# Kernel tuning notes

Measured on AMD Instinct MI355X. Metric: run time of the kernel, lower is better.

Reference implementation:

```python
import jax, jax.numpy as jnp
import numpy as np

FG_THRESH = 0.5
BG_HI = 0.5
BG_LO = 0.0
CLS_LAMBDA = 1.0
BBOX2D_LAMBDA = 1.0
BBOX3D_LAMBDA = 1.0

A, FH, FW, STRIDE = 36, 32, 106, 16  # 36*32*106 = 122112 anchors
B, G, NC = 4, 64, 4


def _smooth_l1(x):
    ax = jnp.abs(x)
    return jnp.where(ax < 1.0, 0.5 * ax * ax, ax - 0.5)


def setup_inputs() -> dict:
    rng = np.random.RandomState(0)
    # anchors: [x1,y1,x2,y2, z, w3d, h3d, l3d, ry], centered at origin
    ws = rng.uniform(16, 256, A).astype(np.float32)
    hs = rng.uniform(16, 256, A).astype(np.float32)
    anchors = np.zeros((A, 9), np.float32)
    anchors[:, 0] = -ws / 2; anchors[:, 1] = -hs / 2
    anchors[:, 2] = ws / 2;  anchors[:, 3] = hs / 2
    anchors[:, 4] = rng.uniform(5, 50, A)
    anchors[:, 5:8] = rng.uniform(1, 5, (A, 3))
    anchors[:, 8] = rng.uniform(-np.pi, np.pi, A)
    # rois = anchors tiled over the feature grid (locate_anchors), col 4 = anchor idx
    sx, sy = np.meshgrid(np.arange(FW) * STRIDE, np.arange(FH) * STRIDE)
    shifts = np.stack([sx.ravel(), sy.ravel(), sx.ravel(), sy.ravel()], 1).astype(np.float32)
    N = FH * FW * A
    rois = np.zeros((N, 5), np.float32)
    rois[:, :4] = (shifts[:, None, :] + anchors[None, :, :4]).reshape(-1, 4)
    rois[:, 4] = np.tile(np.arange(A), FH * FW)
    # GT 2D boxes (x1,y1,x2,y2) inside the 1696x512 image
    gcx = rng.uniform(0, FW * STRIDE, (B, G)); gcy = rng.uniform(0, FH * STRIDE, (B, G))
    gw = rng.uniform(30, 200, (B, G)); gh = rng.uniform(30, 200, (B, G))
    gt_boxes = np.stack([gcx - gw / 2, gcy - gh / 2, gcx + gw / 2, gcy + gh / 2], -1).astype(np.float32)
    # GT 3D: projected 3D center (u,v), z, w3d, h3d, l3d, ry
    gt_boxes_3d = np.stack([
        gcx, gcy,
        rng.uniform(5, 50, (B, G)),
        rng.uniform(1, 5, (B, G)), rng.uniform(1, 5, (B, G)), rng.uniform(1, 5, (B, G)),
        rng.uniform(-np.pi, np.pi, (B, G)),
    ], -1).astype(np.float32)
    gt_labels = rng.randint(1, NC, (B, G)).astype(np.int32)
    bbox_means = (rng.randn(1, 11) * 0.01).astype(np.float32)
    bbox_stds = (0.1 + rng.rand(1, 11) * 0.2).astype(np.float32)
    key = jax.random.key(0)
    k1, k2, k3, k4 = jax.random.split(key, 4)
    return {
        "cls": jax.random.normal(k1, (B, N, NC), jnp.float32),
        "prob": jax.random.uniform(k2, (B, N, NC), jnp.float32),
        "bbox_2d": 0.1 * jax.random.normal(k3, (B, N, 4), jnp.float32),
        "bbox_3d": 0.1 * jax.random.normal(k4, (B, N, 7), jnp.float32),
        "rois": jnp.asarray(rois),
        "anchors": jnp.asarray(anchors),
        "bbox_means": jnp.asarray(bbox_means),
        "bbox_stds": jnp.asarray(bbox_stds),
        "gt_boxes": jnp.asarray(gt_boxes),
        "gt_boxes_3d": jnp.asarray(gt_boxes_3d),
        "gt_labels": jnp.asarray(gt_labels),
    }


def _loss(cls, prob, bbox_2d, bbox_3d, rois, anchors, bbox_means, bbox_stds,
          gt_boxes, gt_boxes_3d, gt_labels):
    # anchor geometry (the +1.0 convention matches the torch code)
    widths = rois[:, 2] - rois[:, 0] + 1.0          # [N]
    heights = rois[:, 3] - rois[:, 1] + 1.0
    ctr_x = rois[:, 0] + 0.5 * widths
    ctr_y = rois[:, 1] + 0.5 * heights
    aidx = rois[:, 4].astype(jnp.int32)
    src = anchors[aidx]                             # [N,9] gathered anchors

    # IoU between every roi and every GT: [B,N,G]
    rx1 = rois[None, :, None, 0]; ry1 = rois[None, :, None, 1]
    rx2 = rois[None, :, None, 2]; ry2 = rois[None, :, None, 3]
    gx1 = gt_boxes[:, None, :, 0]; gy1 = gt_boxes[:, None, :, 1]
    gx2 = gt_boxes[:, None, :, 2]; gy2 = gt_boxes[:, None, :, 3]
    iw = jnp.clip(jnp.minimum(rx2, gx2) - jnp.maximum(rx1, gx1) + 1.0, 0.0)
    ih = jnp.clip(jnp.minimum(ry2, gy2) - jnp.maximum(ry1, gy1) + 1.0, 0.0)
    inter = iw * ih
    area_r = (rx2 - rx1 + 1.0) * (ry2 - ry1 + 1.0)
    area_g = (gx2 - gx1 + 1.0) * (gy2 - gy1 + 1.0)
    ols = inter / (area_r + area_g - inter)         # [B,N,G]

    best_iou = jnp.max(ols, axis=-1)                # [B,N]
    best_gt = jnp.argmax(ols, axis=-1)              # [B,N]

    fg = best_iou >= FG_THRESH
    bg = (best_iou < BG_HI) & (best_iou >= BG_LO) & (~fg)

    matched_lbl = jnp.take_along_axis(gt_labels, best_gt, axis=1)   # [B,N]
    labels = jnp.where(fg, matched_lbl, 0)

    gb = jnp.take_along_axis(gt_boxes, best_gt[..., None], axis=1)  # [B,N,4]
    gw = gb[..., 2] - gb[..., 0] + 1.0
    gh = gb[..., 3] - gb[..., 1] + 1.0
    gcx = gb[..., 0] + 0.5 * gw
    gcy = gb[..., 1] + 0.5 * gh
    t2d = jnp.stack([
        (gcx - ctr_x) / widths,
        (gcy - ctr_y) / heights,
        jnp.log(gw / widths),
        jnp.log(gh / heights),
    ], -1)
    t2d = (t2d - bbox_means[0, 0:4]) / bbox_stds[0, 0:4]

    g3 = jnp.take_along_axis(gt_boxes_3d, best_gt[..., None], axis=1)  # [B,N,7]
    t3d = jnp.stack([
        (g3[..., 0] - ctr_x) / widths,
        (g3[..., 1] - ctr_y) / heights,
        g3[..., 2] - src[:, 4],
        jnp.log(g3[..., 3] / src[:, 5]),
        jnp.log(g3[..., 4] / src[:, 6]),
        jnp.log(g3[..., 5] / src[:, 7]),
        g3[..., 6] - src[:, 8],
    ], -1)
    t3d = (t3d - bbox_means[0, 4:11]) / bbox_stds[0, 4:11]

    # ---- losses
    w_fg = fg.astype(cls.dtype)
    n_fg = jnp.maximum(jnp.sum(w_fg), 1.0)
    loss_b2d = jnp.sum(jnp.sum(_smooth_l1(bbox_2d - t2d), -1) * w_fg) / n_fg
    loss_b3d = jnp.sum(jnp.sum(_smooth_l1(bbox_3d - t3d), -1) * w_fg) / n_fg

    w_cls = (fg | bg).astype(cls.dtype)
    logp = jax.nn.log_softmax(cls, axis=-1)
    ce = -jnp.take_along_axis(logp, labels[..., None], axis=-1)[..., 0]
    loss_cls = jnp.sum(ce * w_cls) / jnp.maximum(jnp.sum(w_cls), 1.0)

    return CLS_LAMBDA * loss_cls + BBOX2D_LAMBDA * loss_b2d + BBOX3D_LAMBDA * loss_b3d


def reference(cls, prob, bbox_2d, bbox_3d, rois, anchors, bbox_means, bbox_stds,
              gt_boxes, gt_boxes_3d, gt_labels):
    return _loss(cls, prob, bbox_2d, bbox_3d, rois, anchors, bbox_means, bbox_stds,
                 gt_boxes, gt_boxes_3d, gt_labels)
```

## Files before the change

### kernel.cpp

```cpp
#include <hip/hip_runtime.h>
#include <math.h>

#define AA 36
#define FWW 106
#define NTOT 122112
#define BB 4
#define GG 64
#define STRIDE_PX 16
#define FBIG 3.402823466e+38f

constexpr int BLOCK = 512;
constexpr int NW    = BLOCK / 64;
constexpr int BLOCKS_PER_B = (NTOT + BLOCK - 1) / BLOCK;
constexpr int NBLK = BB * BLOCKS_PER_B;

__device__ __forceinline__ float smooth_l1(float x) {
    float ax = fabsf(x);
    return (ax < 1.0f) ? 0.5f * ax * ax : ax - 0.5f;
}
__device__ __forceinline__ float frcp(float x) { return __builtin_amdgcn_rcpf(x); }

#define DPP_SELF(x, ctrl, rm)                                                 \
    __int_as_float(__builtin_amdgcn_update_dpp(__float_as_int(x),             \
                   __float_as_int(x), ctrl, rm, 0xf, false))
#define DPP_ZERO(x, ctrl, rm)                                                 \
    __int_as_float(__builtin_amdgcn_update_dpp(0, __float_as_int(x),          \
                   ctrl, rm, 0xf, true))
#define RLANE_F(v, l) __int_as_float(__builtin_amdgcn_readlane(__float_as_int(v), (l)))

__device__ __forceinline__ float wave_sum64(float x) {
    x += DPP_ZERO(x, 0x111, 0xf);
    x += DPP_ZERO(x, 0x112, 0xf);
    x += DPP_ZERO(x, 0x114, 0xf);
    x += DPP_ZERO(x, 0x118, 0xf);
    x += DPP_ZERO(x, 0x142, 0xa);
    x += DPP_ZERO(x, 0x143, 0xc);
    return x;
}
__device__ __forceinline__ float wave_min64_bcast(float x) {
    x = fminf(x, DPP_SELF(x, 0x111, 0xf));
    x = fminf(x, DPP_SELF(x, 0x112, 0xf));
    x = fminf(x, DPP_SELF(x, 0x114, 0xf));
    x = fminf(x, DPP_SELF(x, 0x118, 0xf));
    x = fminf(x, DPP_SELF(x, 0x142, 0xa));
    x = fminf(x, DPP_SELF(x, 0x143, 0xc));
    return RLANE_F(x, 63);
}
__device__ __forceinline__ float wave_max64_bcast(float x) {
    x = fmaxf(x, DPP_SELF(x, 0x111, 0xf));
    x = fmaxf(x, DPP_SELF(x, 0x112, 0xf));
    x = fmaxf(x, DPP_SELF(x, 0x114, 0xf));
    x = fmaxf(x, DPP_SELF(x, 0x118, 0xf));
    x = fmaxf(x, DPP_SELF(x, 0x142, 0xa));
    x = fmaxf(x, DPP_SELF(x, 0x143, 0xc));
    return RLANE_F(x, 63);
}

__global__ __launch_bounds__(BLOCK) void rpn_loss_main(
    const float* __restrict__ cls,
    const float* __restrict__ bbox2d,
    const float* __restrict__ bbox3d,
    const float* __restrict__ anchors,
    const float* __restrict__ means,
    const float* __restrict__ stds,
    const float* __restrict__ gt_boxes,
    const float* __restrict__ gt3d,
    const int*   __restrict__ gt_labels,
    float4* __restrict__ part)
{
    __shared__ float4 s_red[NW];

    const int tid  = threadIdx.x;
    const int lane = tid & 63;
    const int wv   = tid >> 6;
    const int b    = blockIdx.x / BLOCKS_PER_B;
    const int bpos = blockIdx.x % BLOCKS_PER_B;
    const int n0   = bpos * BLOCK;
    const int n    = n0 + tid;
    const bool valid = (n < NTOT);

    const float4* __restrict__ gtb = reinterpret_cast<const float4*>(gt_boxes) + b * GG;

    const size_t row = (size_t)b * NTOT + n;
    float4 c = make_float4(0.f, 0.f, 0.f, 0.f);
    if (valid) c = reinterpret_cast<const float4*>(cls)[row];

    const int aidx  = n % AA;
    const int shift = n / AA;
    const float sx  = (float)((shift % FWW) * STRIDE_PX);
    const float sy  = (float)((shift / FWW) * STRIDE_PX);
    const float a0 = anchors[aidx * 9 + 0];
    const float a1 = anchors[aidx * 9 + 1];
    const float a2 = anchors[aidx * 9 + 2];
    const float a3 = anchors[aidx * 9 + 3];
    const float aw  = a2 - a0 + 1.0f;
    const float ah  = a3 - a1 + 1.0f;
    const float x1  = sx + a0;
    const float y1  = sy + a1;
    const float x2p = x1 + aw;
    const float y2p = y1 + ah;
    const float ar  = aw * ah;

    const float4 gt   = gtb[lane];
    const float  gz1p = gt.z + 1.0f;
    const float  gw1p = gt.w + 1.0f;
    const float  ag   = (gz1p - gt.x) * (gw1p - gt.y);

    float e0 = FBIG, e1 = FBIG, e2 = -FBIG, e3 = -FBIG, ew = 0.f, eh = 0.f, eS = FBIG;
    if (lane < AA) {
        const float b0 = anchors[lane * 9 + 0];
        const float b1 = anchors[lane * 9 + 1];
        const float b2 = anchors[lane * 9 + 2];
        const float b3 = anchors[lane * 9 + 3];
        e0 = b0; e1 = b1; e2 = b2; e3 = b3;
        ew = b2 - b0 + 1.0f;
        eh = b3 - b1 + 1.0f;
        eS = ew * eh;
    }
    const float mnx = wave_min64_bcast(e0);
    const float mny = wave_min64_bcast(e1);
    const float mxx = wave_max64_bcast(e2);
    const float mxy = wave_max64_bcast(e3);
    const float mxw = wave_max64_bcast(ew) + 1.0f;
    const float mxh = wave_max64_bcast(eh) + 1.0f;
    const float mnS = wave_min64_bcast(eS);

    const int nlast = (n0 + BLOCK - 1 < NTOT) ? (n0 + BLOCK - 1) : (NTOT - 1);
    const int s0  = n0 / AA,  s1  = nlast / AA;
    const int sy0 = s0 / FWW, sy1 = s1 / FWW;
    float fxA0, fxA1, fyA, fxB0, fxB1, fyB;
    if (sy0 == sy1) {
        fxA0 = (float)((s0 % FWW) * STRIDE_PX); fxA1 = (float)((s1 % FWW) * STRIDE_PX);
        fyA  = (float)(sy0 * STRIDE_PX);
        fxB0 = fxA0; fxB1 = fxA1; fyB = fyA;
    } else {
        fxA0 = (float)((s0 % FWW) * STRIDE_PX); fxA1 = (float)((FWW - 1) * STRIDE_PX);
        fyA  = (float)(sy0 * STRIDE_PX);
        fxB0 = 0.0f;                            fxB1 = (float)((s1 % FWW) * STRIDE_PX);
        fyB  = (float)(sy1 * STRIDE_PX);
    }

    float iwA = fminf(fxA1 + mxx + 1.0f, gz1p) - fmaxf(fxA0 + mnx, gt.x);
    iwA = fmaxf(fminf(iwA, mxw), 0.0f);
    float ihA = fminf(fyA + mxy + 1.0f, gw1p) - fmaxf(fyA + mny, gt.y);
    ihA = fmaxf(fminf(ihA, mxh), 0.0f);
    bool pass = (3.0f * iwA * ihA >= mnS + ag);
    float iwB = fminf(fxB1 + mxx + 1.0f, gz1p) - fmaxf(fxB0 + mnx, gt.x);
    iwB = fmaxf(fminf(iwB, mxw), 0.0f);
    float ihB = fminf(fyB + mxy + 1.0f, gw1p) - fmaxf(fyB + mny, gt.y);
    ihB = fmaxf(fminf(ihB, mxh), 0.0f);
    pass = pass || (3.0f * iwB * ihB >= mnS + ag);

    unsigned long long m = __ballot(pass);

    const float lse = __logf(__expf(c.x) + __expf(c.y) + __expf(c.z) + __expf(c.w));

    float bi = 0.0f, bS = 1.0f;
    int   bk = 0;
    while (m) {
        const int g = (int)__builtin_ctzll(m);
        m &= (m - 1ull);
        const float gxs = RLANE_F(gt.x,  g);
        const float gys = RLANE_F(gt.y,  g);
        const float gzs = RLANE_F(gz1p,  g);
        const float gws = RLANE_F(gw1p,  g);
        const float ags = RLANE_F(ag,    g);
        const float iw = fminf(x2p, gzs) - fmaxf(x1, gxs);
        const float ih = fmaxf(fminf(y2p, gws) - fmaxf(y1, gys), 0.0f);
        const float inter = iw * ih;
        const float S     = ar + ags;
        const bool upd = inter * bS > bi * S;
        bi = upd ? inter : bi;
        bS = upd ? S     : bS;
        bk = upd ? g     : bk;
    }
    const bool fg = valid && (3.0f * bi >= bS);

    int label = 0;
    if (fg) label = gt_labels[b * GG + bk];
    const float csel = (label == 0) ? c.x : (label == 1) ? c.y :
                       (label == 2) ? c.z : c.w;
    const float ce = valid ? (lse - csel) : 0.0f;

    float l23 = 0.0f;
    if (fg) {
        const float cx  = x1 + 0.5f * aw;
        const float cy  = y1 + 0.5f * ah;
        const float rw  = frcp(aw);
        const float rh  = frcp(ah);
        const float4 gq = gtb[bk];
        const float gw_ = gq.z - gq.x + 1.0f;
        const float gh_ = gq.w - gq.y + 1.0f;
        const float gcx = gq.x + 0.5f * gw_;
        const float gcy = gq.y + 0.5f * gh_;
        float t2[4];
        t2[0] = (gcx - cx) * rw;
        t2[1] = (gcy - cy) * rh;
        t2[2] = __logf(gw_ * rw);
        t2[3] = __logf(gh_ * rh);
        const float4 p2 = reinterpret_cast<const float4*>(bbox2d)[row];
        const float p2a[4] = {p2.x, p2.y, p2.z, p2.w};
        #pragma unroll
        for (int k = 0; k < 4; ++k)
            l23 += smooth_l1(p2a[k] - (t2[k] - means[k]) * frcp(stds[k]));

        const float an4 = anchors[aidx * 9 + 4];
        const float an5 = anchors[aidx * 9 + 5];
        const float an6 = anchors[aidx * 9 + 6];
        const float an7 = anchors[aidx * 9 + 7];
        const float an8 = anchors[aidx * 9 + 8];
        const float* g3 = gt3d + ((size_t)b * GG + bk) * 7;
        float t3[7];
        t3[0] = (g3[0] - cx) * rw;
        t3[1] = (g3[1] - cy) * rh;
        t3[2] = g3[2] - an4;
        t3[3] = __logf(g3[3] * frcp(an5));
        t3[4] = __logf(g3[4] * frcp(an6));
        t3[5] = __logf(g3[5] * frcp(an7));
        t3[6] = g3[6] - an8;
        const float* p3 = bbox3d + row * 7;
        #pragma unroll
        for (int k = 0; k < 7; ++k)
            l23 += smooth_l1(p3[k] - (t3[k] - means[4 + k]) * frcp(stds[4 + k]));
    }

    const float vce = wave_sum64(ce);
    const float vl  = wave_sum64(l23);
    const float nfgw = (float)__popcll(__ballot(fg));
    if (lane == 63) s_red[wv] = make_float4(vce, vl, nfgw, 0.f);
    __syncthreads();
    if (tid < NW) {
        float4 p = s_red[tid];
        #pragma unroll
        for (int mm = 1; mm < NW; mm <<= 1) {
            p.x += __shfl_xor(p.x, mm, 64);
            p.y += __shfl_xor(p.y, mm, 64);
            p.z += __shfl_xor(p.z, mm, 64);
        }
        if (tid == 0) part[blockIdx.x] = p;
    }
}

__global__ __launch_bounds__(256) void rpn_loss_fin(
    const float4* __restrict__ part, float* __restrict__ out)
{
    __shared__ float4 sh[4];
    float ce = 0.f, l23 = 0.f, nfg = 0.f;
    for (int i = threadIdx.x; i < NBLK; i += 256) {
        const float4 p = part[i];
        ce += p.x; l23 += p.y; nfg += p.z;
    }
    ce  = wave_sum64(ce);
    l23 = wave_sum64(l23);
    nfg = wave_sum64(nfg);
    const int lane = threadIdx.x & 63;
    const int wv   = threadIdx.x >> 6;
    if (lane == 63) sh[wv] = make_float4(ce, l23, nfg, 0.f);
    __syncthreads();
    if (threadIdx.x == 0) {
        float a = 0.f, l = 0.f, g = 0.f;
        #pragma unroll
        for (int i = 0; i < 4; ++i) { a += sh[i].x; l += sh[i].y; g += sh[i].z; }
        out[0] = a / (float)((size_t)BB * NTOT) + l / fmaxf(g, 1.0f);
    }
}

extern "C" void kernel_launch(void* const* d_in, const int* in_sizes, int n_in,
                              void* d_out, int out_size, void* d_ws, size_t ws_size,
                              hipStream_t stream) {
    const float* cls     = (const float*)d_in[0];
    const float* bbox2d  = (const float*)d_in[2];
    const float* bbox3d  = (const float*)d_in[3];
    const float* anchors = (const float*)d_in[5];
    const float* means   = (const float*)d_in[6];
    const float* stds    = (const float*)d_in[7];
    const float* gtb     = (const float*)d_in[8];
    const float* gt3     = (const float*)d_in[9];
    const int*   glbl    = (const int*)d_in[10];
    float4* part = (float4*)d_ws;
    float*  out  = (float*)d_out;

    rpn_loss_main<<<dim3(NBLK), BLOCK, 0, stream>>>(cls, bbox2d, bbox3d, anchors,
                                                    means, stds, gtb, gt3, glbl, part);
    rpn_loss_fin<<<1, 256, 0, stream>>>(part, out);
}
```

Measured before the change: 19.15 us.

## Precompute per-block GT candidate masks with per-anchor bounds in a prune kernel

Adds a separate prune kernel that, for each main-kernel block, tests every GT box against each of the 36 anchors over the block's spatial window. It writes a 64-bit candidate mask to workspace, and the main kernel reads that mask instead of computing a loose bound from the min/max envelope of all anchors. Tighter per-anchor bounds should leave fewer GT boxes in the per-thread IoU loop. In exchange it adds a third kernel launch and a global round trip for the masks.

Result: slower. 20.75 us (+8.4%).

```diff
diff --git a/kernel.cpp b/kernel.cpp
--- a/kernel.cpp
+++ b/kernel.cpp
@@ -7,12 +7,13 @@
 #define BB 4
 #define GG 64
 #define STRIDE_PX 16
-#define FBIG 3.402823466e+38f
 
 constexpr int BLOCK = 512;
 constexpr int NW    = BLOCK / 64;
 constexpr int BLOCKS_PER_B = (NTOT + BLOCK - 1) / BLOCK;
 constexpr int NBLK = BB * BLOCKS_PER_B;
+constexpr int PR_BLOCK = 512;
+constexpr int PR_GRID  = (NBLK * 64 + PR_BLOCK - 1) / PR_BLOCK;
 
 __device__ __forceinline__ float smooth_l1(float x) {
     float ax = fabsf(x);
@@ -20,9 +21,6 @@
 }
 __device__ __forceinline__ float frcp(float x) { return __builtin_amdgcn_rcpf(x); }
 
-#define DPP_SELF(x, ctrl, rm)                                                 \
-    __int_as_float(__builtin_amdgcn_update_dpp(__float_as_int(x),             \
-                   __float_as_int(x), ctrl, rm, 0xf, false))
 #define DPP_ZERO(x, ctrl, rm)                                                 \
     __int_as_float(__builtin_amdgcn_update_dpp(0, __float_as_int(x),          \
                    ctrl, rm, 0xf, true))
@@ -37,23 +35,66 @@
     x += DPP_ZERO(x, 0x143, 0xc);
     return x;
 }
-__device__ __forceinline__ float wave_min64_bcast(float x) {
-    x = fminf(x, DPP_SELF(x, 0x111, 0xf));
-    x = fminf(x, DPP_SELF(x, 0x112, 0xf));
-    x = fminf(x, DPP_SELF(x, 0x114, 0xf));
-    x = fminf(x, DPP_SELF(x, 0x118, 0xf));
-    x = fminf(x, DPP_SELF(x, 0x142, 0xa));
-    x = fminf(x, DPP_SELF(x, 0x143, 0xc));
-    return RLANE_F(x, 63);
-}
-__device__ __forceinline__ float wave_max64_bcast(float x) {
-    x = fmaxf(x, DPP_SELF(x, 0x111, 0xf));
-    x = fmaxf(x, DPP_SELF(x, 0x112, 0xf));
-    x = fmaxf(x, DPP_SELF(x, 0x114, 0xf));
-    x = fmaxf(x, DPP_SELF(x, 0x118, 0xf));
-    x = fmaxf(x, DPP_SELF(x, 0x142, 0xa));
-    x = fmaxf(x, DPP_SELF(x, 0x143, 0xc));
-    return RLANE_F(x, 63);
+
+__device__ __forceinline__ void block_windows(int n0,
+    float& fxA0, float& fxA1, float& fyA,
+    float& fxB0, float& fxB1, float& fyB)
+{
+    const int nlast = (n0 + BLOCK - 1 < NTOT) ? (n0 + BLOCK - 1) : (NTOT - 1);
+    const int s0  = n0 / AA,  s1  = nlast / AA;
+    const int sy0 = s0 / FWW, sy1 = s1 / FWW;
+    if (sy0 == sy1) {
+        fxA0 = (float)((s0 % FWW) * STRIDE_PX); fxA1 = (float)((s1 % FWW) * STRIDE_PX);
+        fyA  = (float)(sy0 * STRIDE_PX);
+        fxB0 = fxA0; fxB1 = fxA1; fyB = fyA;
+    } else {
+        fxA0 = (float)((s0 % FWW) * STRIDE_PX); fxA1 = (float)((FWW - 1) * STRIDE_PX);
+        fyA  = (float)(sy0 * STRIDE_PX);
+        fxB0 = 0.0f;                            fxB1 = (float)((s1 % FWW) * STRIDE_PX);
+        fyB  = (float)(sy1 * STRIDE_PX);
+    }
+}
+
+__global__ __launch_bounds__(PR_BLOCK) void rpn_prune(
+    const float* __restrict__ anchors,
+    const float* __restrict__ gt_boxes,
+    unsigned long long* __restrict__ masks)
+{
+    const int gthread = blockIdx.x * PR_BLOCK + threadIdx.x;
+    const int vb   = gthread >> 6;
+    const int lane = threadIdx.x & 63;
+    if (vb >= NBLK) return;
+
+    const int b    = vb / BLOCKS_PER_B;
+    const int bpos = vb % BLOCKS_PER_B;
+    float fxA0, fxA1, fyA, fxB0, fxB1, fyB;
+    block_windows(bpos * BLOCK, fxA0, fxA1, fyA, fxB0, fxB1, fyB);
+
+    const float4 gt = reinterpret_cast<const float4*>(gt_boxes)[b * GG + lane];
+    const float gz1p = gt.z + 1.0f;
+    const float gw1p = gt.w + 1.0f;
+    const float ag   = (gz1p - gt.x) * (gw1p - gt.y);
+
+    bool pass = false;
+    for (int a = 0; a < AA; ++a) {
+        const float ax1 = anchors[a * 9 + 0];
+        const float ay1 = anchors[a * 9 + 1];
+        const float aw  = anchors[a * 9 + 2] - ax1 + 1.0f;
+        const float ah  = anchors[a * 9 + 3] - ay1 + 1.0f;
+        const float thr = aw * ah + ag;
+        float iwA = fminf(fxA1 + ax1 + aw, gz1p) - fmaxf(fxA0 + ax1, gt.x);
+        float ihA = fminf(fyA  + ay1 + ah, gw1p) - fmaxf(fyA  + ay1, gt.y);
+        iwA = fmaxf(fminf(iwA, aw), 0.0f);
+        ihA = fmaxf(fminf(ihA, ah), 0.0f);
+        pass |= (3.0f * iwA * ihA >= thr);
+        float iwB = fminf(fxB1 + ax1 + aw, gz1p) - fmaxf(fxB0 + ax1, gt.x);
+        float ihB = fminf(fyB  + ay1 + ah, gw1p) - fmaxf(fyB  + ay1, gt.y);
+        iwB = fmaxf(fminf(iwB, aw), 0.0f);
+        ihB = fmaxf(fminf(ihB, ah), 0.0f);
+        pass |= (3.0f * iwB * ihB >= thr);
+    }
+    const unsigned long long m = __ballot(pass);
+    if (lane == 0) masks[vb] = m;
 }
 
 __global__ __launch_bounds__(BLOCK) void rpn_loss_main(
@@ -66,6 +107,7 @@
     const float* __restrict__ gt_boxes,
     const float* __restrict__ gt3d,
     const int*   __restrict__ gt_labels,
+    const unsigned long long* __restrict__ masks,
     float4* __restrict__ part)
 {
     __shared__ float4 s_red[NW];
@@ -84,6 +126,13 @@
     const size_t row = (size_t)b * NTOT + n;
     float4 c = make_float4(0.f, 0.f, 0.f, 0.f);
     if (valid) c = reinterpret_cast<const float4*>(cls)[row];
+
+    unsigned long long m = masks[blockIdx.x];
+
+    const float4 gt   = gtb[lane];
+    const float  gz1p = gt.z + 1.0f;
+    const float  gw1p = gt.w + 1.0f;
+    const float  ag   = (gz1p - gt.x) * (gw1p - gt.y);
 
     const int aidx  = n % AA;
     const int shift = n / AA;
@@ -101,58 +150,6 @@
     const float y2p = y1 + ah;
     const float ar  = aw * ah;
 
-    const float4 gt   = gtb[lane];
-    const float  gz1p = gt.z + 1.0f;
-    const float  gw1p = gt.w + 1.0f;
-    const float  ag   = (gz1p - gt.x) * (gw1p - gt.y);
-
-    float e0 = FBIG, e1 = FBIG, e2 = -FBIG, e3 = -FBIG, ew = 0.f, eh = 0.f, eS = FBIG;
-    if (lane < AA) {
-        const float b0 = anchors[lane * 9 + 0];
-        const float b1 = anchors[lane * 9 + 1];
-        const float b2 = anchors[lane * 9 + 2];
-        const float b3 = anchors[lane * 9 + 3];
-        e0 = b0; e1 = b1; e2 = b2; e3 = b3;
-        ew = b2 - b0 + 1.0f;
-        eh = b3 - b1 + 1.0f;
-        eS = ew * eh;
-    }
-    const float mnx = wave_min64_bcast(e0);
-    const float mny = wave_min64_bcast(e1);
-    const float mxx = wave_max64_bcast(e2);
-    const float mxy = wave_max64_bcast(e3);
-    const float mxw = wave_max64_bcast(ew) + 1.0f;
-    const float mxh = wave_max64_bcast(eh) + 1.0f;
-    const float mnS = wave_min64_bcast(eS);
-
-    const int nlast = (n0 + BLOCK - 1 < NTOT) ? (n0 + BLOCK - 1) : (NTOT - 1);
-    const int s0  = n0 / AA,  s1  = nlast / AA;
-    const int sy0 = s0 / FWW, sy1 = s1 / FWW;
-    float fxA0, fxA1, fyA, fxB0, fxB1, fyB;
-    if (sy0 == sy1) {
-        fxA0 = (float)((s0 % FWW) * STRIDE_PX); fxA1 = (float)((s1 % FWW) * STRIDE_PX);
-        fyA  = (float)(sy0 * STRIDE_PX);
-        fxB0 = fxA0; fxB1 = fxA1; fyB = fyA;
-    } else {
-        fxA0 = (float)((s0 % FWW) * STRIDE_PX); fxA1 = (float)((FWW - 1) * STRIDE_PX);
-        fyA  = (float)(sy0 * STRIDE_PX);
-        fxB0 = 0.0f;                            fxB1 = (float)((s1 % FWW) * STRIDE_PX);
-        fyB  = (float)(sy1 * STRIDE_PX);
-    }
-
-    float iwA = fminf(fxA1 + mxx + 1.0f, gz1p) - fmaxf(fxA0 + mnx, gt.x);
-    iwA = fmaxf(fminf(iwA, mxw), 0.0f);
-    float ihA = fminf(fyA + mxy + 1.0f, gw1p) - fmaxf(fyA + mny, gt.y);
-    ihA = fmaxf(fminf(ihA, mxh), 0.0f);
-    bool pass = (3.0f * iwA * ihA >= mnS + ag);
-    float iwB = fminf(fxB1 + mxx + 1.0f, gz1p) - fmaxf(fxB0 + mnx, gt.x);
-    iwB = fmaxf(fminf(iwB, mxw), 0.0f);
-    float ihB = fminf(fyB + mxy + 1.0f, gw1p) - fmaxf(fyB + mny, gt.y);
-    ihB = fmaxf(fminf(ihB, mxh), 0.0f);
-    pass = pass || (3.0f * iwB * ihB >= mnS + ag);
-
-    unsigned long long m = __ballot(pass);
-
     const float lse = __logf(__expf(c.x) + __expf(c.y) + __expf(c.z) + __expf(c.w));
 
     float bi = 0.0f, bS = 1.0f;
@@ -160,11 +157,11 @@
     while (m) {
         const int g = (int)__builtin_ctzll(m);
         m &= (m - 1ull);
-        const float gxs = RLANE_F(gt.x,  g);
-        const float gys = RLANE_F(gt.y,  g);
-        const float gzs = RLANE_F(gz1p,  g);
-        const float gws = RLANE_F(gw1p,  g);
-        const float ags = RLANE_F(ag,    g);
+        const float gxs = RLANE_F(gt.x, g);
+        const float gys = RLANE_F(gt.y, g);
+        const float gzs = RLANE_F(gz1p, g);
+        const float gws = RLANE_F(gw1p, g);
+        const float ags = RLANE_F(ag,   g);
         const float iw = fminf(x2p, gzs) - fmaxf(x1, gxs);
         const float ih = fmaxf(fminf(y2p, gws) - fmaxf(y1, gys), 0.0f);
         const float inter = iw * ih;
@@ -277,10 +274,14 @@
     const float* gtb     = (const float*)d_in[8];
     const float* gt3     = (const float*)d_in[9];
     const int*   glbl    = (const int*)d_in[10];
+
     float4* part = (float4*)d_ws;
+    unsigned long long* masks = (unsigned long long*)(part + NBLK);
     float*  out  = (float*)d_out;
 
+    rpn_prune<<<dim3(PR_GRID), PR_BLOCK, 0, stream>>>(anchors, gtb, masks);
     rpn_loss_main<<<dim3(NBLK), BLOCK, 0, stream>>>(cls, bbox2d, bbox3d, anchors,
-                                                    means, stds, gtb, gt3, glbl, part);
+                                                    means, stds, gtb, gt3, glbl,
+                                                    masks, part);
     rpn_loss_fin<<<1, 256, 0, stream>>>(part, out);
 }
```
